# Kernel optimization log

Hardware: AMD Instinct MI355X
Metric: run time of the kernel (lower is better)

Reference implementation:

```python
import jax, jax.numpy as jnp
import numpy as np

N_NODES = 100000
N_EDGES = 1600000
D_NODE = 32
D_EDGE = 16
D_HID = 64
D_OUT = 32


def setup_inputs() -> dict:
    key = jax.random.key(0)
    ks = jax.random.split(key, 7)
    x = jax.random.normal(ks[0], (N_NODES, D_NODE), dtype=jnp.float32)
    edge_index = jax.random.randint(ks[1], (2, N_EDGES), 0, N_NODES, dtype=jnp.int64)
    edge_attr = jax.random.normal(ks[2], (N_EDGES, D_EDGE), dtype=jnp.float32)
    # 2-layer MLP params (Linear -> ReLU -> Linear), He-ish scaling
    W1 = jax.random.normal(ks[3], (D_NODE + D_EDGE, D_HID), dtype=jnp.float32) * (2.0 / (D_NODE + D_EDGE)) ** 0.5
    b1 = jnp.zeros((D_HID,), dtype=jnp.float32)
    W2 = jax.random.normal(ks[4], (D_HID, D_OUT), dtype=jnp.float32) * (2.0 / D_HID) ** 0.5
    b2 = jnp.zeros((D_OUT,), dtype=jnp.float32)
    return {"x": x, "edge_index": edge_index, "edge_attr": edge_attr,
            "W1": W1, "b1": b1, "W2": W2, "b2": b2}


def reference(x, edge_index, edge_attr, W1, b1, W2, b2):
    row, col = edge_index[0], edge_index[1]
    # gather source-node feats and concat with edge feats: [E, d_node + d_edge]
    inp = jnp.concatenate([x[col], edge_attr], axis=1)
    # 2-layer MLP over edges
    h = jax.nn.relu(inp @ W1 + b1)
    messages = h @ W2 + b2  # [E, d_out]
    # scatter-sum aggregate by destination node
    message = jax.ops.segment_sum(messages, row, num_segments=x.shape[0])
    return message
```

## Files before the change

### kernel.cpp

```cpp
#include <hip/hip_runtime.h>
#include <hip/hip_bf16.h>
#include <stdint.h>

#define N_NODES 100000
#define N_EDGES 1600000
#define D_NODE  32
#define D_EDGE  16
#define D_IN    48
#define D_HID   64
#define D_OUT   32

#define NFLAGS_OFF  ((size_t)0)
#define NB1_OFF     ((size_t)64)
#define NB2_OFF     ((size_t)320)
#define W1BF_OFF    ((size_t)1024)
#define W2BF_OFF    ((size_t)9216)
#define COUNTS_OFF  ((size_t)65536)
#define OFFSETS_OFF ((size_t)466944)
#define BLKSUM_OFF  ((size_t)917504)
#define RANK_OFF    ((size_t)1048576)
#define MSG_OFF     ((size_t)8388608)

#define SCAN_NB 391

typedef __attribute__((ext_vector_type(8))) short bf16x8;
typedef __attribute__((ext_vector_type(4))) float f32x4;

__device__ inline float bf2f(unsigned int u16) {
    return __uint_as_float(u16 << 16);
}
__device__ inline unsigned short f2bf_rne(float f) {
    unsigned int x = __float_as_uint(f);
    unsigned int r = (x + 0x7FFFu + ((x >> 16) & 1u)) >> 16;
    return (unsigned short)r;
}
__device__ inline unsigned int pk_bf2(float a, float b) {
    float2 f; f.x = a; f.y = b;
    __hip_bfloat162 h = __float22bfloat162_rn(f);
    return *reinterpret_cast<unsigned int*>(&h);
}
__device__ inline float ld_f(const void* p, int i, int isbf) {
    if (isbf) return bf2f(((const unsigned short*)p)[i]);
    return ((const float*)p)[i];
}
__device__ inline bf16x8 pack_bf8(float4 v0, float4 v1) {
    union { unsigned int u[4]; bf16x8 v; } r;
    r.u[0] = pk_bf2(v0.x, v0.y);
    r.u[1] = pk_bf2(v0.z, v0.w);
    r.u[2] = pk_bf2(v1.x, v1.y);
    r.u[3] = pk_bf2(v1.z, v1.w);
    return r.v;
}

__global__ __launch_bounds__(256) void prep_kernel(
        const void* __restrict__ xq, const void* __restrict__ idxq,
        const void* __restrict__ W1q, const void* __restrict__ b1q,
        const void* __restrict__ W2q, const void* __restrict__ b2q,
        char* __restrict__ ws) {
    const int t = threadIdx.x;
    const int i0 = blockIdx.x * 256 + t;
    int* counts = (int*)(ws + COUNTS_OFF);
    if (i0 < N_NODES) counts[i0] = 0;
    if (blockIdx.x != 0) return;

    __shared__ int s_isbf;
    if (t < 64) {
        unsigned short u = ((const unsigned short*)xq)[t];
        unsigned long long mb = __ballot(((u >> 7) & 0xFF) >= 140);
        int wodd = ((const int*)idxq)[2 * t + 1];
        unsigned long long mi = __ballot(wodd != 0);
        if (t == 0) {
            int* flags = (int*)(ws + NFLAGS_OFF);
            flags[0] = (mb == 0ULL);
            flags[1] = (mi == 0ULL);
            s_isbf = (mb == 0ULL);
        }
    }
    __syncthreads();
    const int isbf = s_isbf;
    float* b1 = (float*)(ws + NB1_OFF);
    float* b2 = (float*)(ws + NB2_OFF);
    unsigned short* w1b = (unsigned short*)(ws + W1BF_OFF);
    unsigned short* w2b = (unsigned short*)(ws + W2BF_OFF);

    if (t < D_HID) b1[t] = ld_f(b1q, t, isbf);
    if (t < D_OUT) b2[t] = ld_f(b2q, t, isbf);

    for (int i = t; i < D_HID * 64; i += 256) {
        int n = i >> 6, k = i & 63;
        float v = (k < D_IN) ? ld_f(W1q, k * D_HID + n, isbf) : 0.0f;
        w1b[i] = f2bf_rne(v);
    }
    for (int i = t; i < D_OUT * 64; i += 256) {
        int n = i >> 6, k = i & 63;
        w2b[i] = f2bf_rne(ld_f(W2q, k * D_OUT + n, isbf));
    }
}

__global__ __launch_bounds__(256) void hist_kernel(const void* __restrict__ idxq,
                                                   char* __restrict__ ws,
                                                   int* __restrict__ rankb) {
    const int is64 = ((const int*)(ws + NFLAGS_OFF))[1];
    const int e = blockIdx.x * 256 + threadIdx.x;
    int dst;
    if (is64) dst = (int)((const long long*)idxq)[e];
    else      dst = ((const int*)idxq)[e];
    rankb[e] = atomicAdd((int*)(ws + COUNTS_OFF) + dst, 1);
}

__global__ __launch_bounds__(256) void scan_block_kernel(char* __restrict__ ws) {
    __shared__ int s[256];
    const int* counts = (const int*)(ws + COUNTS_OFF);
    int* offs   = (int*)(ws + OFFSETS_OFF);
    int* blksum = (int*)(ws + BLKSUM_OFF);
    const int t = threadIdx.x;
    const int i = blockIdx.x * 256 + t;
    int v = (i < N_NODES) ? counts[i] : 0;
    s[t] = v;
    __syncthreads();
    for (int d = 1; d < 256; d <<= 1) {
        int a = (t >= d) ? s[t - d] : 0;
        __syncthreads();
        s[t] += a;
        __syncthreads();
    }
    if (i < N_NODES) offs[i] = s[t] - v;
    if (t == 255) blksum[blockIdx.x] = s[255];
}

__global__ __launch_bounds__(256) void scan_add_kernel(char* __restrict__ ws) {
    __shared__ int s[256];
    int* offs = (int*)(ws + OFFSETS_OFF);
    const int* blksum = (const int*)(ws + BLKSUM_OFF);
    const int t = threadIdx.x;
    const int b = blockIdx.x;
    int acc = 0;
    for (int j = t; j < b; j += 256) acc += blksum[j];
    s[t] = acc;
    __syncthreads();
    for (int d = 128; d > 0; d >>= 1) {
        if (t < d) s[t] += s[t + d];
        __syncthreads();
    }
    const int prefix = s[0];
    const int i = b * 256 + t;
    if (i < N_NODES) offs[i] += prefix;
    if (i == 0) offs[N_NODES] = N_EDGES;
}

__global__ __launch_bounds__(256) void edge_mlp_mfma_kernel(
        const void* __restrict__ xq,
        const void* __restrict__ idxq,
        const void* __restrict__ eaq,
        const char* __restrict__ wsro,
        const int* __restrict__ rankb,
        unsigned short* __restrict__ msg) {
    const int isbf = ((const int*)(wsro + NFLAGS_OFF))[0];
    const int is64 = ((const int*)(wsro + NFLAGS_OFF))[1];

    __shared__ __align__(16) unsigned short hbuf[4][2][16][72];

    const int w   = threadIdx.x >> 6;
    const int l   = threadIdx.x & 63;
    const int m16 = l & 15;
    const int q   = l >> 4;

    const unsigned short* w1b = (const unsigned short*)(wsro + W1BF_OFF);
    const unsigned short* w2b = (const unsigned short*)(wsro + W2BF_OFF);
    const float* b1 = (const float*)(wsro + NB1_OFF);
    const float* b2 = (const float*)(wsro + NB2_OFF);
    const int* offs = (const int*)(wsro + OFFSETS_OFF);

    bf16x8 w1f[4][2], w2f[2][2];
#pragma unroll
    for (int t = 0; t < 4; ++t)
#pragma unroll
        for (int c = 0; c < 2; ++c)
            w1f[t][c] = *(const bf16x8*)(w1b + ((t * 16 + m16) * 64 + c * 32 + q * 8));
#pragma unroll
    for (int t = 0; t < 2; ++t)
#pragma unroll
        for (int c = 0; c < 2; ++c)
            w2f[t][c] = *(const bf16x8*)(w2b + ((t * 16 + m16) * 64 + c * 32 + q * 8));

    const int eb = blockIdx.x * 256 + w * 64;

    int srcv[4], posv[4];
#pragma unroll
    for (int g = 0; g < 4; ++g) {
        const int e = eb + g * 16 + m16;
        int dst;
        if (is64) {
            const long long* ip = (const long long*)idxq;
            dst = (int)ip[e];
            srcv[g] = (int)ip[N_EDGES + e];
        } else {
            const int* ip = (const int*)idxq;
            dst = ip[e];
            srcv[g] = ip[N_EDGES + e];
        }
        posv[g] = offs[dst] + rankb[e];
    }

    bf16x8 A0[4], A1[4];
#pragma unroll
    for (int g = 0; g < 4; ++g) {
        const int e = eb + g * 16 + m16;
        if (isbf) {
            const unsigned short* x  = (const unsigned short*)xq;
            const unsigned short* ea = (const unsigned short*)eaq;
            A0[g] = *(const bf16x8*)(x + (size_t)srcv[g] * D_NODE + q * 8);
            A1[g] = *(const bf16x8*)(ea + (size_t)e * D_EDGE + (q & 1) * 8);
        } else {
            const float* x  = (const float*)xq;
            const float* ea = (const float*)eaq;
            const float4* xp = (const float4*)(x + (size_t)srcv[g] * D_NODE + q * 8);
            A0[g] = pack_bf8(xp[0], xp[1]);
            const float4* ap = (const float4*)(ea + (size_t)e * D_EDGE + (q & 1) * 8);
            A1[g] = pack_bf8(ap[0], ap[1]);
        }
    }

    const float b1v[4] = { b1[m16], b1[16 + m16], b1[32 + m16], b1[48 + m16] };
    const float b2v[2] = { b2[m16], b2[16 + m16] };
    const int mrow = l >> 2;
    const int sub  = l & 3;

    auto L1 = [&](int g, int b) {
#pragma unroll
        for (int t = 0; t < 4; ++t) {
            f32x4 c;
            c[0] = c[1] = c[2] = c[3] = b1v[t];
            c = __builtin_amdgcn_mfma_f32_16x16x32_bf16(A0[g], w1f[t][0], c, 0, 0, 0);
            c = __builtin_amdgcn_mfma_f32_16x16x32_bf16(A1[g], w1f[t][1], c, 0, 0, 0);
            unsigned int u0 = pk_bf2(fmaxf(c[0], 0.0f), fmaxf(c[1], 0.0f));
            unsigned int u1 = pk_bf2(fmaxf(c[2], 0.0f), fmaxf(c[3], 0.0f));
            hbuf[w][b][q * 4 + 0][t * 16 + m16] = (unsigned short)u0;
            hbuf[w][b][q * 4 + 1][t * 16 + m16] = (unsigned short)(u0 >> 16);
            hbuf[w][b][q * 4 + 2][t * 16 + m16] = (unsigned short)u1;
            hbuf[w][b][q * 4 + 3][t * 16 + m16] = (unsigned short)(u1 >> 16);
        }
    };
    auto L2S = [&](int g, int b) {
        bf16x8 a20 = *(const bf16x8*)(&hbuf[w][b][m16][q * 8]);
        bf16x8 a21 = *(const bf16x8*)(&hbuf[w][b][m16][32 + q * 8]);
#pragma unroll
        for (int t = 0; t < 2; ++t) {
            f32x4 c;
            c[0] = c[1] = c[2] = c[3] = b2v[t];
            c = __builtin_amdgcn_mfma_f32_16x16x32_bf16(a20, w2f[t][0], c, 0, 0, 0);
            c = __builtin_amdgcn_mfma_f32_16x16x32_bf16(a21, w2f[t][1], c, 0, 0, 0);
            unsigned int u0 = pk_bf2(c[0], c[1]);
            unsigned int u1 = pk_bf2(c[2], c[3]);
            hbuf[w][b][q * 4 + 0][t * 16 + m16] = (unsigned short)u0;
            hbuf[w][b][q * 4 + 1][t * 16 + m16] = (unsigned short)(u0 >> 16);
            hbuf[w][b][q * 4 + 2][t * 16 + m16] = (unsigned short)u1;
            hbuf[w][b][q * 4 + 3][t * 16 + m16] = (unsigned short)(u1 >> 16);
        }
        const int posm = __shfl(posv[g], mrow, 64);
        uint4 rowv = *(const uint4*)(&hbuf[w][b][mrow][sub * 8]);
        *(uint4*)(msg + (size_t)posm * D_OUT + sub * 8) = rowv;
    };

    L1(0, 0);
    L1(1, 1);
    L2S(0, 0);
    L1(2, 0);
    L2S(1, 1);
    L1(3, 1);
    L2S(2, 0);
    L2S(3, 1);
}

__global__ __launch_bounds__(256) void reduce_kernel(
        const char* __restrict__ wsro, const unsigned short* __restrict__ msg,
        void* __restrict__ out) {
    const int isbf = ((const int*)(wsro + NFLAGS_OFF))[0];
    const int* offs = (const int*)(wsro + OFFSETS_OFF);
    const int t = blockIdx.x * 256 + threadIdx.x;
    const int node = t >> 4;
    if (node >= N_NODES) return;
    const int c2 = t & 15;
    const int lo = offs[node], hi = offs[node + 1];
    float s0 = 0.0f, s1 = 0.0f;
    const unsigned int* p = (const unsigned int*)msg + (size_t)lo * 16 + c2;
    int k = lo;
    for (; k + 1 < hi; k += 2) {
        unsigned int a = p[0], b = p[16];
        s0 += __uint_as_float(a << 16) + __uint_as_float(b << 16);
        s1 += __uint_as_float(a & 0xFFFF0000u) + __uint_as_float(b & 0xFFFF0000u);
        p += 32;
    }
    if (k < hi) {
        unsigned int a = p[0];
        s0 += __uint_as_float(a << 16);
        s1 += __uint_as_float(a & 0xFFFF0000u);
    }
    if (isbf) {
        ((unsigned int*)out)[(size_t)node * 16 + c2] = pk_bf2(s0, s1);
    } else {
        float2 v; v.x = s0; v.y = s1;
        ((float2*)out)[(size_t)node * 16 + c2] = v;
    }
}

extern "C" void kernel_launch(void* const* d_in, const int* in_sizes, int n_in,
                              void* d_out, int out_size, void* d_ws, size_t ws_size,
                              hipStream_t stream) {
    const void* x   = d_in[0];
    const void* idx = d_in[1];
    const void* ea  = d_in[2];
    const void* W1  = d_in[3];
    const void* b1  = d_in[4];
    const void* W2  = d_in[5];
    const void* b2  = d_in[6];
    char* ws = (char*)d_ws;

    hipLaunchKernelGGL(prep_kernel, dim3(SCAN_NB), dim3(256), 0, stream,
                       x, idx, W1, b1, W2, b2, ws);

    hipLaunchKernelGGL(hist_kernel, dim3(N_EDGES / 256), dim3(256), 0, stream,
                       idx, ws, (int*)(ws + RANK_OFF));

    hipLaunchKernelGGL(scan_block_kernel, dim3(SCAN_NB), dim3(256), 0, stream, ws);
    hipLaunchKernelGGL(scan_add_kernel,   dim3(SCAN_NB), dim3(256), 0, stream, ws);

    hipLaunchKernelGGL(edge_mlp_mfma_kernel, dim3(N_EDGES / 256), dim3(256), 0, stream,
                       x, idx, ea, (const char*)ws,
                       (const int*)(ws + RANK_OFF), (unsigned short*)(ws + MSG_OFF));

    hipLaunchKernelGGL(reduce_kernel, dim3((N_NODES * 16 + 255) / 256), dim3(256), 0, stream,
                       (const char*)ws, (const unsigned short*)(ws + MSG_OFF), d_out);
}
```

Before: 369.4 us.

## Prefetch edge inputs one group ahead and reduce each node with a full wavefront

The edge MLP kernel no longer loads all four groups of gathered node and edge features up front. It now runs a non-unrolled loop that loads the next group while computing the current one, and uses a single LDS buffer per wave instead of two. This lowers register and LDS pressure to raise occupancy, at the cost of less interleaving between groups. The reduce kernel now gives each node a 64-lane wave that reads 16 message rows at a time with 16-byte loads and combines them with xor shuffles. This replaces 16 threads reading 4-byte words row by row, but wastes lanes on nodes with few edges (average degree is 16).

```diff
diff --git a/kernel.cpp b/kernel.cpp
--- a/kernel.cpp
+++ b/kernel.cpp
@@ -158,7 +158,7 @@
     const int isbf = ((const int*)(wsro + NFLAGS_OFF))[0];
     const int is64 = ((const int*)(wsro + NFLAGS_OFF))[1];
 
-    __shared__ __align__(16) unsigned short hbuf[4][2][16][72];
+    __shared__ __align__(16) unsigned short hbuf[4][16][72];
 
     const int w   = threadIdx.x >> 6;
     const int l   = threadIdx.x & 63;
@@ -202,48 +202,51 @@
         posv[g] = offs[dst] + rankb[e];
     }
 
-    bf16x8 A0[4], A1[4];
-#pragma unroll
-    for (int g = 0; g < 4; ++g) {
+    const float b1v[4] = { b1[m16], b1[16 + m16], b1[32 + m16], b1[48 + m16] };
+    const float b2v[2] = { b2[m16], b2[16 + m16] };
+    const int mrow = l >> 2;
+    const int sub  = l & 3;
+
+    auto loadA = [&](int g, bf16x8& a0, bf16x8& a1) {
         const int e = eb + g * 16 + m16;
         if (isbf) {
             const unsigned short* x  = (const unsigned short*)xq;
             const unsigned short* ea = (const unsigned short*)eaq;
-            A0[g] = *(const bf16x8*)(x + (size_t)srcv[g] * D_NODE + q * 8);
-            A1[g] = *(const bf16x8*)(ea + (size_t)e * D_EDGE + (q & 1) * 8);
+            a0 = *(const bf16x8*)(x + (size_t)srcv[g] * D_NODE + q * 8);
+            a1 = *(const bf16x8*)(ea + (size_t)e * D_EDGE + (q & 1) * 8);
         } else {
             const float* x  = (const float*)xq;
             const float* ea = (const float*)eaq;
             const float4* xp = (const float4*)(x + (size_t)srcv[g] * D_NODE + q * 8);
-            A0[g] = pack_bf8(xp[0], xp[1]);
+            a0 = pack_bf8(xp[0], xp[1]);
             const float4* ap = (const float4*)(ea + (size_t)e * D_EDGE + (q & 1) * 8);
-            A1[g] = pack_bf8(ap[0], ap[1]);
-        }
-    }
-
-    const float b1v[4] = { b1[m16], b1[16 + m16], b1[32 + m16], b1[48 + m16] };
-    const float b2v[2] = { b2[m16], b2[16 + m16] };
-    const int mrow = l >> 2;
-    const int sub  = l & 3;
-
-    auto L1 = [&](int g, int b) {
+            a1 = pack_bf8(ap[0], ap[1]);
+        }
+    };
+
+    bf16x8 A0c, A1c, A0n, A1n;
+    loadA(0, A0c, A1c);
+
+#pragma unroll 1
+    for (int g = 0; g < 4; ++g) {
+        if (g < 3) loadA(g + 1, A0n, A1n);
+
 #pragma unroll
         for (int t = 0; t < 4; ++t) {
             f32x4 c;
             c[0] = c[1] = c[2] = c[3] = b1v[t];
-            c = __builtin_amdgcn_mfma_f32_16x16x32_bf16(A0[g], w1f[t][0], c, 0, 0, 0);
-            c = __builtin_amdgcn_mfma_f32_16x16x32_bf16(A1[g], w1f[t][1], c, 0, 0, 0);
+            c = __builtin_amdgcn_mfma_f32_16x16x32_bf16(A0c, w1f[t][0], c, 0, 0, 0);
+            c = __builtin_amdgcn_mfma_f32_16x16x32_bf16(A1c, w1f[t][1], c, 0, 0, 0);
             unsigned int u0 = pk_bf2(fmaxf(c[0], 0.0f), fmaxf(c[1], 0.0f));
             unsigned int u1 = pk_bf2(fmaxf(c[2], 0.0f), fmaxf(c[3], 0.0f));
-            hbuf[w][b][q * 4 + 0][t * 16 + m16] = (unsigned short)u0;
-            hbuf[w][b][q * 4 + 1][t * 16 + m16] = (unsigned short)(u0 >> 16);
-            hbuf[w][b][q * 4 + 2][t * 16 + m16] = (unsigned short)u1;
-            hbuf[w][b][q * 4 + 3][t * 16 + m16] = (unsigned short)(u1 >> 16);
-        }
-    };
-    auto L2S = [&](int g, int b) {
-        bf16x8 a20 = *(const bf16x8*)(&hbuf[w][b][m16][q * 8]);
-        bf16x8 a21 = *(const bf16x8*)(&hbuf[w][b][m16][32 + q * 8]);
+            hbuf[w][q * 4 + 0][t * 16 + m16] = (unsigned short)u0;
+            hbuf[w][q * 4 + 1][t * 16 + m16] = (unsigned short)(u0 >> 16);
+            hbuf[w][q * 4 + 2][t * 16 + m16] = (unsigned short)u1;
+            hbuf[w][q * 4 + 3][t * 16 + m16] = (unsigned short)(u1 >> 16);
+        }
+
+        bf16x8 a20 = *(const bf16x8*)(&hbuf[w][m16][q * 8]);
+        bf16x8 a21 = *(const bf16x8*)(&hbuf[w][m16][32 + q * 8]);
 #pragma unroll
         for (int t = 0; t < 2; ++t) {
             f32x4 c;
@@ -252,24 +255,18 @@
             c = __builtin_amdgcn_mfma_f32_16x16x32_bf16(a21, w2f[t][1], c, 0, 0, 0);
             unsigned int u0 = pk_bf2(c[0], c[1]);
             unsigned int u1 = pk_bf2(c[2], c[3]);
-            hbuf[w][b][q * 4 + 0][t * 16 + m16] = (unsigned short)u0;
-            hbuf[w][b][q * 4 + 1][t * 16 + m16] = (unsigned short)(u0 >> 16);
-            hbuf[w][b][q * 4 + 2][t * 16 + m16] = (unsigned short)u1;
-            hbuf[w][b][q * 4 + 3][t * 16 + m16] = (unsigned short)(u1 >> 16);
-        }
+            hbuf[w][q * 4 + 0][t * 16 + m16] = (unsigned short)u0;
+            hbuf[w][q * 4 + 1][t * 16 + m16] = (unsigned short)(u0 >> 16);
+            hbuf[w][q * 4 + 2][t * 16 + m16] = (unsigned short)u1;
+            hbuf[w][q * 4 + 3][t * 16 + m16] = (unsigned short)(u1 >> 16);
+        }
+
         const int posm = __shfl(posv[g], mrow, 64);
-        uint4 rowv = *(const uint4*)(&hbuf[w][b][mrow][sub * 8]);
+        uint4 rowv = *(const uint4*)(&hbuf[w][mrow][sub * 8]);
         *(uint4*)(msg + (size_t)posm * D_OUT + sub * 8) = rowv;
-    };
-
-    L1(0, 0);
-    L1(1, 1);
-    L2S(0, 0);
-    L1(2, 0);
-    L2S(1, 1);
-    L1(3, 1);
-    L2S(2, 0);
-    L2S(3, 1);
+
+        A0c = A0n; A1c = A1n;
+    }
 }
 
 __global__ __launch_bounds__(256) void reduce_kernel(
@@ -277,30 +274,45 @@
         void* __restrict__ out) {
     const int isbf = ((const int*)(wsro + NFLAGS_OFF))[0];
     const int* offs = (const int*)(wsro + OFFSETS_OFF);
-    const int t = blockIdx.x * 256 + threadIdx.x;
-    const int node = t >> 4;
+    const int node = (blockIdx.x * 256 + threadIdx.x) >> 6;
     if (node >= N_NODES) return;
-    const int c2 = t & 15;
+    const int l   = threadIdx.x & 63;
+    const int r   = l >> 2;
+    const int sub = l & 3;
+
     const int lo = offs[node], hi = offs[node + 1];
-    float s0 = 0.0f, s1 = 0.0f;
-    const unsigned int* p = (const unsigned int*)msg + (size_t)lo * 16 + c2;
-    int k = lo;
-    for (; k + 1 < hi; k += 2) {
-        unsigned int a = p[0], b = p[16];
-        s0 += __uint_as_float(a << 16) + __uint_as_float(b << 16);
-        s1 += __uint_as_float(a & 0xFFFF0000u) + __uint_as_float(b & 0xFFFF0000u);
-        p += 32;
-    }
-    if (k < hi) {
-        unsigned int a = p[0];
-        s0 += __uint_as_float(a << 16);
-        s1 += __uint_as_float(a & 0xFFFF0000u);
-    }
-    if (isbf) {
-        ((unsigned int*)out)[(size_t)node * 16 + c2] = pk_bf2(s0, s1);
-    } else {
-        float2 v; v.x = s0; v.y = s1;
-        ((float2*)out)[(size_t)node * 16 + c2] = v;
+    float a0 = 0.f, a1 = 0.f, a2 = 0.f, a3 = 0.f,
+          a4 = 0.f, a5 = 0.f, a6 = 0.f, a7 = 0.f;
+    for (int k = lo; k < hi; k += 16) {
+        const int row = k + r;
+        if (row < hi) {
+            uint4 v = *(const uint4*)(msg + (size_t)row * D_OUT + sub * 8);
+            a0 += __uint_as_float(v.x << 16); a1 += __uint_as_float(v.x & 0xFFFF0000u);
+            a2 += __uint_as_float(v.y << 16); a3 += __uint_as_float(v.y & 0xFFFF0000u);
+            a4 += __uint_as_float(v.z << 16); a5 += __uint_as_float(v.z & 0xFFFF0000u);
+            a6 += __uint_as_float(v.w << 16); a7 += __uint_as_float(v.w & 0xFFFF0000u);
+        }
+    }
+#pragma unroll
+    for (int mask = 4; mask <= 32; mask <<= 1) {
+        a0 += __shfl_xor(a0, mask, 64); a1 += __shfl_xor(a1, mask, 64);
+        a2 += __shfl_xor(a2, mask, 64); a3 += __shfl_xor(a3, mask, 64);
+        a4 += __shfl_xor(a4, mask, 64); a5 += __shfl_xor(a5, mask, 64);
+        a6 += __shfl_xor(a6, mask, 64); a7 += __shfl_xor(a7, mask, 64);
+    }
+    if (r == 0) {
+        if (isbf) {
+            uint4 p;
+            p.x = pk_bf2(a0, a1); p.y = pk_bf2(a2, a3);
+            p.z = pk_bf2(a4, a5); p.w = pk_bf2(a6, a7);
+            *(uint4*)((unsigned short*)out + (size_t)node * D_OUT + sub * 8) = p;
+        } else {
+            float4* op = (float4*)((float*)out + (size_t)node * D_OUT + sub * 8);
+            float4 v0; v0.x = a0; v0.y = a1; v0.z = a2; v0.w = a3;
+            float4 v1; v1.x = a4; v1.y = a5; v1.z = a6; v1.w = a7;
+            op[0] = v0;
+            op[1] = v1;
+        }
     }
 }
 
@@ -329,6 +341,6 @@
                        x, idx, ea, (const char*)ws,
                        (const int*)(ws + RANK_OFF), (unsigned short*)(ws + MSG_OFF));
 
-    hipLaunchKernelGGL(reduce_kernel, dim3((N_NODES * 16 + 255) / 256), dim3(256), 0, stream,
+    hipLaunchKernelGGL(reduce_kernel, dim3((N_NODES + 3) / 4), dim3(256), 0, stream,
                        (const char*)ws, (const unsigned short*)(ws + MSG_OFF), d_out);
 }
```

New measurement: 384.4 us. +4.0%, slower.

## Fuse all stages into one persistent cooperative kernel with grid syncs

Applied to the files above, without the earlier changes.

Adds a persistent cooperative mega_kernel that runs weight prep, histogram, two-pass scan, edge MLP and segment reduce in one launch, separated by grid-wide syncs, with grid-stride loops over a grid sized from occupancy (up to 8 blocks per CU). The aim is to remove the launch gaps between six kernels. The edge MLP in both paths also changes from a double-buffered LDS schedule with all inputs preloaded to a single-buffered loop that prefetches the next group's inputs, which lowers register and LDS use. In exchange, every phase is limited to the resident grid, and the grid syncs plus the smaller grid may cut parallelism in the memory-bound phases. The old multi-kernel path is kept as a fallback.

```diff
diff --git a/kernel.cpp b/kernel.cpp
--- a/kernel.cpp
+++ b/kernel.cpp
@@ -1,12 +1,14 @@
 #include <hip/hip_runtime.h>
 #include <hip/hip_bf16.h>
+#include <hip/hip_cooperative_groups.h>
 #include <stdint.h>
+
+namespace cg = cooperative_groups;
 
 #define N_NODES 100000
 #define N_EDGES 1600000
 #define D_NODE  32
 #define D_EDGE  16
-#define D_IN    48
 #define D_HID   64
 #define D_OUT   32
 
@@ -16,7 +18,7 @@
 #define W1BF_OFF    ((size_t)1024)
 #define W2BF_OFF    ((size_t)9216)
 #define COUNTS_OFF  ((size_t)65536)
-#define OFFSETS_OFF ((size_t)466944)
+#define OFFS_OFF    ((size_t)466944)
 #define BLKSUM_OFF  ((size_t)917504)
 #define RANK_OFF    ((size_t)1048576)
 #define MSG_OFF     ((size_t)8388608)
@@ -52,6 +54,243 @@
     return r.v;
 }
 
+__global__ __launch_bounds__(256) void mega_kernel(
+        const void* __restrict__ xq, const void* __restrict__ idxq,
+        const void* __restrict__ eaq,
+        const void* __restrict__ W1q, const void* __restrict__ b1q,
+        const void* __restrict__ W2q, const void* __restrict__ b2q,
+        char* __restrict__ ws, void* __restrict__ out) {
+    cg::grid_group gridg = cg::this_grid();
+    const int t = threadIdx.x;
+    const int gtid = blockIdx.x * 256 + t;
+    const int gthreads = gridDim.x * 256;
+
+    __shared__ __align__(16) unsigned short hbuf[4][16][72];
+    __shared__ int sscan[256];
+    __shared__ int s_isbf0;
+
+    int* counts = (int*)(ws + COUNTS_OFF);
+    int* offs   = (int*)(ws + OFFS_OFF);
+    int* blksum = (int*)(ws + BLKSUM_OFF);
+    int* rankb  = (int*)(ws + RANK_OFF);
+    unsigned short* msg = (unsigned short*)(ws + MSG_OFF);
+
+    for (int i = gtid; i < N_NODES; i += gthreads) counts[i] = 0;
+    if (blockIdx.x == 0) {
+        if (t < 64) {
+            unsigned short u = ((const unsigned short*)xq)[t];
+            unsigned long long mb = __ballot(((u >> 7) & 0xFF) >= 140);
+            int wodd = ((const int*)idxq)[2 * t + 1];
+            unsigned long long mi = __ballot(wodd != 0);
+            if (t == 0) {
+                int* flags = (int*)(ws + NFLAGS_OFF);
+                flags[0] = (mb == 0ULL);
+                flags[1] = (mi == 0ULL);
+                s_isbf0 = (mb == 0ULL);
+            }
+        }
+        __syncthreads();
+        const int isbf0 = s_isbf0;
+        float* b1 = (float*)(ws + NB1_OFF);
+        float* b2 = (float*)(ws + NB2_OFF);
+        unsigned short* w1b = (unsigned short*)(ws + W1BF_OFF);
+        unsigned short* w2b = (unsigned short*)(ws + W2BF_OFF);
+        if (t < D_HID) b1[t] = ld_f(b1q, t, isbf0);
+        if (t < D_OUT) b2[t] = ld_f(b2q, t, isbf0);
+        for (int i = t; i < D_HID * 64; i += 256) {
+            int n = i >> 6, k = i & 63;
+            float v = (k < 48) ? ld_f(W1q, k * D_HID + n, isbf0) : 0.0f;
+            w1b[i] = f2bf_rne(v);
+        }
+        for (int i = t; i < D_OUT * 64; i += 256) {
+            int n = i >> 6, k = i & 63;
+            w2b[i] = f2bf_rne(ld_f(W2q, k * D_OUT + n, isbf0));
+        }
+    }
+    gridg.sync();
+
+    const int isbf = ((const int*)(ws + NFLAGS_OFF))[0];
+    const int is64 = ((const int*)(ws + NFLAGS_OFF))[1];
+
+    for (int e = gtid; e < N_EDGES; e += gthreads) {
+        int dst;
+        if (is64) dst = (int)((const long long*)idxq)[e];
+        else      dst = ((const int*)idxq)[e];
+        rankb[e] = atomicAdd(counts + dst, 1);
+    }
+    gridg.sync();
+
+    for (int c = blockIdx.x; c < SCAN_NB; c += gridDim.x) {
+        const int i = c * 256 + t;
+        int v = (i < N_NODES) ? counts[i] : 0;
+        sscan[t] = v;
+        __syncthreads();
+        for (int d = 1; d < 256; d <<= 1) {
+            int a = (t >= d) ? sscan[t - d] : 0;
+            __syncthreads();
+            sscan[t] += a;
+            __syncthreads();
+        }
+        if (i < N_NODES) offs[i] = sscan[t] - v;
+        if (t == 255) blksum[c] = sscan[255];
+        __syncthreads();
+    }
+    gridg.sync();
+    for (int c = blockIdx.x; c < SCAN_NB; c += gridDim.x) {
+        int acc = 0;
+        for (int j = t; j < c; j += 256) acc += blksum[j];
+        sscan[t] = acc;
+        __syncthreads();
+        for (int d = 128; d > 0; d >>= 1) {
+            if (t < d) sscan[t] += sscan[t + d];
+            __syncthreads();
+        }
+        const int prefix = sscan[0];
+        const int i = c * 256 + t;
+        if (i < N_NODES) offs[i] += prefix;
+        __syncthreads();
+    }
+    if (gtid == 0) offs[N_NODES] = N_EDGES;
+    gridg.sync();
+
+    {
+        const int w   = t >> 6;
+        const int l   = t & 63;
+        const int m16 = l & 15;
+        const int q   = l >> 4;
+        const unsigned short* w1b = (const unsigned short*)(ws + W1BF_OFF);
+        const unsigned short* w2b = (const unsigned short*)(ws + W2BF_OFF);
+        const float* b1 = (const float*)(ws + NB1_OFF);
+        const float* b2 = (const float*)(ws + NB2_OFF);
+
+        bf16x8 w1f[4][2], w2f[2][2];
+#pragma unroll
+        for (int ti = 0; ti < 4; ++ti)
+#pragma unroll
+            for (int c = 0; c < 2; ++c)
+                w1f[ti][c] = *(const bf16x8*)(w1b + ((ti * 16 + m16) * 64 + c * 32 + q * 8));
+#pragma unroll
+        for (int ti = 0; ti < 2; ++ti)
+#pragma unroll
+            for (int c = 0; c < 2; ++c)
+                w2f[ti][c] = *(const bf16x8*)(w2b + ((ti * 16 + m16) * 64 + c * 32 + q * 8));
+
+        const float b1v[4] = { b1[m16], b1[16 + m16], b1[32 + m16], b1[48 + m16] };
+        const float b2v[2] = { b2[m16], b2[16 + m16] };
+        const int mrow = l >> 2;
+        const int sub  = l & 3;
+
+        auto loadA = [&](int eb_, int g, int src, bf16x8& a0, bf16x8& a1) {
+            const int e = eb_ + g * 16 + m16;
+            if (isbf) {
+                const unsigned short* x  = (const unsigned short*)xq;
+                const unsigned short* ea = (const unsigned short*)eaq;
+                a0 = *(const bf16x8*)(x + (size_t)src * D_NODE + q * 8);
+                a1 = *(const bf16x8*)(ea + (size_t)e * D_EDGE + (q & 1) * 8);
+            } else {
+                const float* x  = (const float*)xq;
+                const float* ea = (const float*)eaq;
+                const float4* xp = (const float4*)(x + (size_t)src * D_NODE + q * 8);
+                a0 = pack_bf8(xp[0], xp[1]);
+                const float4* ap = (const float4*)(ea + (size_t)e * D_EDGE + (q & 1) * 8);
+                a1 = pack_bf8(ap[0], ap[1]);
+            }
+        };
+
+        const int nw  = gridDim.x * 4;
+        const int wid = blockIdx.x * 4 + w;
+        for (int task = wid; task < N_EDGES / 64; task += nw) {
+            const int eb = task * 64;
+            int srcv[4], posv[4];
+#pragma unroll
+            for (int g = 0; g < 4; ++g) {
+                const int e = eb + g * 16 + m16;
+                int dst;
+                if (is64) {
+                    const long long* ip = (const long long*)idxq;
+                    dst = (int)ip[e];
+                    srcv[g] = (int)ip[N_EDGES + e];
+                } else {
+                    const int* ip = (const int*)idxq;
+                    dst = ip[e];
+                    srcv[g] = ip[N_EDGES + e];
+                }
+                posv[g] = offs[dst] + rankb[e];
+            }
+
+            bf16x8 A0c, A1c, A0n, A1n;
+            loadA(eb, 0, srcv[0], A0c, A1c);
+#pragma unroll 1
+            for (int g = 0; g < 4; ++g) {
+                if (g < 3) loadA(eb, g + 1, srcv[g + 1], A0n, A1n);
+
+#pragma unroll
+                for (int ti = 0; ti < 4; ++ti) {
+                    f32x4 c;
+                    c[0] = c[1] = c[2] = c[3] = b1v[ti];
+                    c = __builtin_amdgcn_mfma_f32_16x16x32_bf16(A0c, w1f[ti][0], c, 0, 0, 0);
+                    c = __builtin_amdgcn_mfma_f32_16x16x32_bf16(A1c, w1f[ti][1], c, 0, 0, 0);
+                    unsigned int u0 = pk_bf2(fmaxf(c[0], 0.0f), fmaxf(c[1], 0.0f));
+                    unsigned int u1 = pk_bf2(fmaxf(c[2], 0.0f), fmaxf(c[3], 0.0f));
+                    hbuf[w][q * 4 + 0][ti * 16 + m16] = (unsigned short)u0;
+                    hbuf[w][q * 4 + 1][ti * 16 + m16] = (unsigned short)(u0 >> 16);
+                    hbuf[w][q * 4 + 2][ti * 16 + m16] = (unsigned short)u1;
+                    hbuf[w][q * 4 + 3][ti * 16 + m16] = (unsigned short)(u1 >> 16);
+                }
+
+                bf16x8 a20 = *(const bf16x8*)(&hbuf[w][m16][q * 8]);
+                bf16x8 a21 = *(const bf16x8*)(&hbuf[w][m16][32 + q * 8]);
+#pragma unroll
+                for (int ti = 0; ti < 2; ++ti) {
+                    f32x4 c;
+                    c[0] = c[1] = c[2] = c[3] = b2v[ti];
+                    c = __builtin_amdgcn_mfma_f32_16x16x32_bf16(a20, w2f[ti][0], c, 0, 0, 0);
+                    c = __builtin_amdgcn_mfma_f32_16x16x32_bf16(a21, w2f[ti][1], c, 0, 0, 0);
+                    unsigned int u0 = pk_bf2(c[0], c[1]);
+                    unsigned int u1 = pk_bf2(c[2], c[3]);
+                    hbuf[w][q * 4 + 0][ti * 16 + m16] = (unsigned short)u0;
+                    hbuf[w][q * 4 + 1][ti * 16 + m16] = (unsigned short)(u0 >> 16);
+                    hbuf[w][q * 4 + 2][ti * 16 + m16] = (unsigned short)u1;
+                    hbuf[w][q * 4 + 3][ti * 16 + m16] = (unsigned short)(u1 >> 16);
+                }
+
+                const int posm = __shfl(posv[g], mrow, 64);
+                uint4 rowv = *(const uint4*)(&hbuf[w][mrow][sub * 8]);
+                *(uint4*)(msg + (size_t)posm * D_OUT + sub * 8) = rowv;
+
+                A0c = A0n; A1c = A1n;
+            }
+        }
+    }
+    gridg.sync();
+
+    for (int ii = gtid; ii < N_NODES * 16; ii += gthreads) {
+        const int node = ii >> 4;
+        const int c2 = ii & 15;
+        const int lo = offs[node], hi = offs[node + 1];
+        float s0 = 0.0f, s1 = 0.0f;
+        const unsigned int* p = (const unsigned int*)msg + (size_t)lo * 16 + c2;
+        int k = lo;
+        for (; k + 1 < hi; k += 2) {
+            unsigned int a = p[0], b = p[16];
+            s0 += __uint_as_float(a << 16) + __uint_as_float(b << 16);
+            s1 += __uint_as_float(a & 0xFFFF0000u) + __uint_as_float(b & 0xFFFF0000u);
+            p += 32;
+        }
+        if (k < hi) {
+            unsigned int a = p[0];
+            s0 += __uint_as_float(a << 16);
+            s1 += __uint_as_float(a & 0xFFFF0000u);
+        }
+        if (isbf) {
+            ((unsigned int*)out)[(size_t)node * 16 + c2] = pk_bf2(s0, s1);
+        } else {
+            float2 v; v.x = s0; v.y = s1;
+            ((float2*)out)[(size_t)node * 16 + c2] = v;
+        }
+    }
+}
+
 __global__ __launch_bounds__(256) void prep_kernel(
         const void* __restrict__ xq, const void* __restrict__ idxq,
         const void* __restrict__ W1q, const void* __restrict__ b1q,
@@ -59,10 +298,8 @@
         char* __restrict__ ws) {
     const int t = threadIdx.x;
     const int i0 = blockIdx.x * 256 + t;
-    int* counts = (int*)(ws + COUNTS_OFF);
-    if (i0 < N_NODES) counts[i0] = 0;
+    if (i0 < N_NODES) ((int*)(ws + COUNTS_OFF))[i0] = 0;
     if (blockIdx.x != 0) return;
-
     __shared__ int s_isbf;
     if (t < 64) {
         unsigned short u = ((const unsigned short*)xq)[t];
@@ -82,13 +319,11 @@
     float* b2 = (float*)(ws + NB2_OFF);
     unsigned short* w1b = (unsigned short*)(ws + W1BF_OFF);
     unsigned short* w2b = (unsigned short*)(ws + W2BF_OFF);
-
     if (t < D_HID) b1[t] = ld_f(b1q, t, isbf);
     if (t < D_OUT) b2[t] = ld_f(b2q, t, isbf);
-
     for (int i = t; i < D_HID * 64; i += 256) {
         int n = i >> 6, k = i & 63;
-        float v = (k < D_IN) ? ld_f(W1q, k * D_HID + n, isbf) : 0.0f;
+        float v = (k < 48) ? ld_f(W1q, k * D_HID + n, isbf) : 0.0f;
         w1b[i] = f2bf_rne(v);
     }
     for (int i = t; i < D_OUT * 64; i += 256) {
@@ -111,7 +346,7 @@
 __global__ __launch_bounds__(256) void scan_block_kernel(char* __restrict__ ws) {
     __shared__ int s[256];
     const int* counts = (const int*)(ws + COUNTS_OFF);
-    int* offs   = (int*)(ws + OFFSETS_OFF);
+    int* offs   = (int*)(ws + OFFS_OFF);
     int* blksum = (int*)(ws + BLKSUM_OFF);
     const int t = threadIdx.x;
     const int i = blockIdx.x * 256 + t;
@@ -130,7 +365,7 @@
 
 __global__ __launch_bounds__(256) void scan_add_kernel(char* __restrict__ ws) {
     __shared__ int s[256];
-    int* offs = (int*)(ws + OFFSETS_OFF);
+    int* offs = (int*)(ws + OFFS_OFF);
     const int* blksum = (const int*)(ws + BLKSUM_OFF);
     const int t = threadIdx.x;
     const int b = blockIdx.x;
@@ -157,34 +392,28 @@
         unsigned short* __restrict__ msg) {
     const int isbf = ((const int*)(wsro + NFLAGS_OFF))[0];
     const int is64 = ((const int*)(wsro + NFLAGS_OFF))[1];
-
-    __shared__ __align__(16) unsigned short hbuf[4][2][16][72];
-
+    __shared__ __align__(16) unsigned short hbuf[4][16][72];
     const int w   = threadIdx.x >> 6;
     const int l   = threadIdx.x & 63;
     const int m16 = l & 15;
     const int q   = l >> 4;
-
     const unsigned short* w1b = (const unsigned short*)(wsro + W1BF_OFF);
     const unsigned short* w2b = (const unsigned short*)(wsro + W2BF_OFF);
     const float* b1 = (const float*)(wsro + NB1_OFF);
     const float* b2 = (const float*)(wsro + NB2_OFF);
-    const int* offs = (const int*)(wsro + OFFSETS_OFF);
-
+    const int* offs = (const int*)(wsro + OFFS_OFF);
     bf16x8 w1f[4][2], w2f[2][2];
 #pragma unroll
-    for (int t = 0; t < 4; ++t)
+    for (int ti = 0; ti < 4; ++ti)
 #pragma unroll
         for (int c = 0; c < 2; ++c)
-            w1f[t][c] = *(const bf16x8*)(w1b + ((t * 16 + m16) * 64 + c * 32 + q * 8));
-#pragma unroll
-    for (int t = 0; t < 2; ++t)
+            w1f[ti][c] = *(const bf16x8*)(w1b + ((ti * 16 + m16) * 64 + c * 32 + q * 8));
+#pragma unroll
+    for (int ti = 0; ti < 2; ++ti)
 #pragma unroll
         for (int c = 0; c < 2; ++c)
-            w2f[t][c] = *(const bf16x8*)(w2b + ((t * 16 + m16) * 64 + c * 32 + q * 8));
-
+            w2f[ti][c] = *(const bf16x8*)(w2b + ((ti * 16 + m16) * 64 + c * 32 + q * 8));
     const int eb = blockIdx.x * 256 + w * 64;
-
     int srcv[4], posv[4];
 #pragma unroll
     for (int g = 0; g < 4; ++g) {
@@ -201,82 +430,71 @@
         }
         posv[g] = offs[dst] + rankb[e];
     }
-
-    bf16x8 A0[4], A1[4];
-#pragma unroll
-    for (int g = 0; g < 4; ++g) {
+    const float b1v[4] = { b1[m16], b1[16 + m16], b1[32 + m16], b1[48 + m16] };
+    const float b2v[2] = { b2[m16], b2[16 + m16] };
+    const int mrow = l >> 2;
+    const int sub  = l & 3;
+    auto loadA = [&](int g, bf16x8& a0, bf16x8& a1) {
         const int e = eb + g * 16 + m16;
         if (isbf) {
             const unsigned short* x  = (const unsigned short*)xq;
             const unsigned short* ea = (const unsigned short*)eaq;
-            A0[g] = *(const bf16x8*)(x + (size_t)srcv[g] * D_NODE + q * 8);
-            A1[g] = *(const bf16x8*)(ea + (size_t)e * D_EDGE + (q & 1) * 8);
+            a0 = *(const bf16x8*)(x + (size_t)srcv[g] * D_NODE + q * 8);
+            a1 = *(const bf16x8*)(ea + (size_t)e * D_EDGE + (q & 1) * 8);
         } else {
             const float* x  = (const float*)xq;
             const float* ea = (const float*)eaq;
             const float4* xp = (const float4*)(x + (size_t)srcv[g] * D_NODE + q * 8);
-            A0[g] = pack_bf8(xp[0], xp[1]);
+            a0 = pack_bf8(xp[0], xp[1]);
             const float4* ap = (const float4*)(ea + (size_t)e * D_EDGE + (q & 1) * 8);
-            A1[g] = pack_bf8(ap[0], ap[1]);
-        }
-    }
-
-    const float b1v[4] = { b1[m16], b1[16 + m16], b1[32 + m16], b1[48 + m16] };
-    const float b2v[2] = { b2[m16], b2[16 + m16] };
-    const int mrow = l >> 2;
-    const int sub  = l & 3;
-
-    auto L1 = [&](int g, int b) {
-#pragma unroll
-        for (int t = 0; t < 4; ++t) {
+            a1 = pack_bf8(ap[0], ap[1]);
+        }
+    };
+    bf16x8 A0c, A1c, A0n, A1n;
+    loadA(0, A0c, A1c);
+#pragma unroll 1
+    for (int g = 0; g < 4; ++g) {
+        if (g < 3) loadA(g + 1, A0n, A1n);
+#pragma unroll
+        for (int ti = 0; ti < 4; ++ti) {
             f32x4 c;
-            c[0] = c[1] = c[2] = c[3] = b1v[t];
-            c = __builtin_amdgcn_mfma_f32_16x16x32_bf16(A0[g], w1f[t][0], c, 0, 0, 0);
-            c = __builtin_amdgcn_mfma_f32_16x16x32_bf16(A1[g], w1f[t][1], c, 0, 0, 0);
+            c[0] = c[1] = c[2] = c[3] = b1v[ti];
+            c = __builtin_amdgcn_mfma_f32_16x16x32_bf16(A0c, w1f[ti][0], c, 0, 0, 0);
+            c = __builtin_amdgcn_mfma_f32_16x16x32_bf16(A1c, w1f[ti][1], c, 0, 0, 0);
             unsigned int u0 = pk_bf2(fmaxf(c[0], 0.0f), fmaxf(c[1], 0.0f));
             unsigned int u1 = pk_bf2(fmaxf(c[2], 0.0f), fmaxf(c[3], 0.0f));
-            hbuf[w][b][q * 4 + 0][t * 16 + m16] = (unsigned short)u0;
-            hbuf[w][b][q * 4 + 1][t * 16 + m16] = (unsigned short)(u0 >> 16);
-            hbuf[w][b][q * 4 + 2][t * 16 + m16] = (unsigned short)u1;
-            hbuf[w][b][q * 4 + 3][t * 16 + m16] = (unsigned short)(u1 >> 16);
-        }
-    };
-    auto L2S = [&](int g, int b) {
-        bf16x8 a20 = *(const bf16x8*)(&hbuf[w][b][m16][q * 8]);
-        bf16x8 a21 = *(const bf16x8*)(&hbuf[w][b][m16][32 + q * 8]);
-#pragma unroll
-        for (int t = 0; t < 2; ++t) {
+            hbuf[w][q * 4 + 0][ti * 16 + m16] = (unsigned short)u0;
+            hbuf[w][q * 4 + 1][ti * 16 + m16] = (unsigned short)(u0 >> 16);
+            hbuf[w][q * 4 + 2][ti * 16 + m16] = (unsigned short)u1;
+            hbuf[w][q * 4 + 3][ti * 16 + m16] = (unsigned short)(u1 >> 16);
+        }
+        bf16x8 a20 = *(const bf16x8*)(&hbuf[w][m16][q * 8]);
+        bf16x8 a21 = *(const bf16x8*)(&hbuf[w][m16][32 + q * 8]);
+#pragma unroll
+        for (int ti = 0; ti < 2; ++ti) {
             f32x4 c;
-            c[0] = c[1] = c[2] = c[3] = b2v[t];
-            c = __builtin_amdgcn_mfma_f32_16x16x32_bf16(a20, w2f[t][0], c, 0, 0, 0);
-            c = __builtin_amdgcn_mfma_f32_16x16x32_bf16(a21, w2f[t][1], c, 0, 0, 0);
+            c[0] = c[1] = c[2] = c[3] = b2v[ti];
+            c = __builtin_amdgcn_mfma_f32_16x16x32_bf16(a20, w2f[ti][0], c, 0, 0, 0);
+            c = __builtin_amdgcn_mfma_f32_16x16x32_bf16(a21, w2f[ti][1], c, 0, 0, 0);
             unsigned int u0 = pk_bf2(c[0], c[1]);
             unsigned int u1 = pk_bf2(c[2], c[3]);
-            hbuf[w][b][q * 4 + 0][t * 16 + m16] = (unsigned short)u0;
-            hbuf[w][b][q * 4 + 1][t * 16 + m16] = (unsigned short)(u0 >> 16);
-            hbuf[w][b][q * 4 + 2][t * 16 + m16] = (unsigned short)u1;
-            hbuf[w][b][q * 4 + 3][t * 16 + m16] = (unsigned short)(u1 >> 16);
+            hbuf[w][q * 4 + 0][ti * 16 + m16] = (unsigned short)u0;
+            hbuf[w][q * 4 + 1][ti * 16 + m16] = (unsigned short)(u0 >> 16);
+            hbuf[w][q * 4 + 2][ti * 16 + m16] = (unsigned short)u1;
+            hbuf[w][q * 4 + 3][ti * 16 + m16] = (unsigned short)(u1 >> 16);
         }
         const int posm = __shfl(posv[g], mrow, 64);
-        uint4 rowv = *(const uint4*)(&hbuf[w][b][mrow][sub * 8]);
+        uint4 rowv = *(const uint4*)(&hbuf[w][mrow][sub * 8]);
         *(uint4*)(msg + (size_t)posm * D_OUT + sub * 8) = rowv;
-    };
-
-    L1(0, 0);
-    L1(1, 1);
-    L2S(0, 0);
-    L1(2, 0);
-    L2S(1, 1);
-    L1(3, 1);
-    L2S(2, 0);
-    L2S(3, 1);
+        A0c = A0n; A1c = A1n;
+    }
 }
 
 __global__ __launch_bounds__(256) void reduce_kernel(
         const char* __restrict__ wsro, const unsigned short* __restrict__ msg,
         void* __restrict__ out) {
     const int isbf = ((const int*)(wsro + NFLAGS_OFF))[0];
-    const int* offs = (const int*)(wsro + OFFSETS_OFF);
+    const int* offs = (const int*)(wsro + OFFS_OFF);
     const int t = blockIdx.x * 256 + threadIdx.x;
     const int node = t >> 4;
     if (node >= N_NODES) return;
@@ -316,19 +534,31 @@
     const void* b2  = d_in[6];
     char* ws = (char*)d_ws;
 
+    int maxB = 0;
+    hipError_t oe = hipOccupancyMaxActiveBlocksPerMultiprocessor(&maxB, mega_kernel, 256, 0);
+    if (oe == hipSuccess && maxB >= 1) {
+        int nb = maxB;
+        if (nb > 8) nb = 8;
+        int grid = nb * 256;
+        void* outp = d_out;
+        void* args[] = { (void*)&x, (void*)&idx, (void*)&ea,
+                         (void*)&W1, (void*)&b1, (void*)&W2, (void*)&b2,
+                         (void*)&ws, (void*)&outp };
+        hipError_t le = hipLaunchCooperativeKernel((void*)mega_kernel,
+                                                   dim3(grid), dim3(256),
+                                                   args, 0, stream);
+        if (le == hipSuccess) return;
+    }
+
     hipLaunchKernelGGL(prep_kernel, dim3(SCAN_NB), dim3(256), 0, stream,
                        x, idx, W1, b1, W2, b2, ws);
-
     hipLaunchKernelGGL(hist_kernel, dim3(N_EDGES / 256), dim3(256), 0, stream,
                        idx, ws, (int*)(ws + RANK_OFF));
-
     hipLaunchKernelGGL(scan_block_kernel, dim3(SCAN_NB), dim3(256), 0, stream, ws);
     hipLaunchKernelGGL(scan_add_kernel,   dim3(SCAN_NB), dim3(256), 0, stream, ws);
-
     hipLaunchKernelGGL(edge_mlp_mfma_kernel, dim3(N_EDGES / 256), dim3(256), 0, stream,
                        x, idx, ea, (const char*)ws,
                        (const int*)(ws + RANK_OFF), (unsigned short*)(ws + MSG_OFF));
-
     hipLaunchKernelGGL(reduce_kernel, dim3((N_NODES * 16 + 255) / 256), dim3(256), 0, stream,
                        (const char*)ws, (const unsigned short*)(ws + MSG_OFF), d_out);
 }
```

New measurement: 644.1 us. 1.74x slower.
